# Kernel tuning notes

Hardware: AMD Instinct MI355X
Metric: run time of the kernel (lower is better)

The kernel has to match this reference:

```python
import jax, jax.numpy as jnp
import numpy as np

B = 4096          # events
L = 524288        # total set points (avg 128 per event)
CIN = 16          # per-point feature size (set feature 'a')
DVEC = 32         # flat feature size (feature 'b')
PHI = [128, 128, 64]
MLP = [256, 128]
EPS = 1e-5        # BatchNorm1d eps


def setup_inputs() -> dict:
    key = jax.random.key(0)
    ks = jax.random.split(key, 10)
    def n(k, shape, scale=0.05):
        return jax.random.normal(k, shape, dtype=jnp.float32) * scale
    return {
        "x_a": jax.random.normal(ks[0], (1, CIN, L), dtype=jnp.float32),
        "x_b": jax.random.normal(ks[1], (B, DVEC), dtype=jnp.float32),
        # row 0 -> counts for set feature 'a'; row 1 ignored (Reshape branch)
        "sample_indices": jnp.full((2, B), L // B, dtype=jnp.int32),
        "W1": n(ks[2], (PHI[0], CIN)),  "b1": jnp.zeros((PHI[0],), jnp.float32),
        "W2": n(ks[3], (PHI[1], PHI[0])), "b2": jnp.zeros((PHI[1],), jnp.float32),
        "W3": n(ks[4], (PHI[2], PHI[1])), "b3": jnp.zeros((PHI[2],), jnp.float32),
        "Wm1": n(ks[5], (MLP[0], PHI[2] + DVEC)), "bm1": jnp.zeros((MLP[0],), jnp.float32),
        "g1": jnp.ones((MLP[0],), jnp.float32), "be1": jnp.zeros((MLP[0],), jnp.float32),
        "Wm2": n(ks[6], (MLP[1], MLP[0])), "bm2": jnp.zeros((MLP[1],), jnp.float32),
        "g2": jnp.ones((MLP[1],), jnp.float32), "be2": jnp.zeros((MLP[1],), jnp.float32),
        "Wm3": n(ks[7], (1, MLP[1])), "bm3": jnp.zeros((1,), jnp.float32),
    }


def _bn(x, g, b):
    # BatchNorm1d, training-mode batch stats, biased variance (torch semantics)
    mu = jnp.mean(x, axis=0)
    var = jnp.var(x, axis=0)
    return (x - mu) * jax.lax.rsqrt(var + EPS) * g + b


def reference(x_a, x_b, sample_indices,
              W1, b1, W2, b2, W3, b3,
              Wm1, bm1, g1, be1, Wm2, bm2, g2, be2, Wm3, bm3):
    counts = sample_indices[0].astype(jnp.int32)                       # [B]
    bounds = jnp.concatenate([jnp.zeros((1,), jnp.int32), jnp.cumsum(counts)])  # [B+1]

    # PhiNet: pointwise Conv1d stack (kernel size 1) on [CIN, L]
    h = x_a[0]
    h = jax.nn.relu(jnp.einsum('oc,cl->ol', W1, h) + b1[:, None])
    h = jax.nn.relu(jnp.einsum('oc,cl->ol', W2, h) + b2[:, None])
    h = jax.nn.relu(jnp.einsum('oc,cl->ol', W3, h) + b3[:, None])      # [64, L]

    # fused segment-mean: point p belongs to segment j iff bounds[j] <= p < bounds[j+1]
    seg = jnp.searchsorted(bounds, jnp.arange(h.shape[1], dtype=jnp.int32), side='right') - 1
    sums = jax.ops.segment_sum(h.T, seg, num_segments=counts.shape[0])  # [B, 64]
    means = sums / jnp.maximum(counts, 1).astype(jnp.float32)[:, None]

    # feature order: sorted keys -> ('a' set repr, 'b' flat)
    z = jnp.concatenate([means, x_b.reshape(-1, DVEC)], axis=1)        # [B, 96]

    z = jax.nn.relu(_bn(z @ Wm1.T + bm1, g1, be1))
    z = jax.nn.relu(_bn(z @ Wm2.T + bm2, g2, be2))
    return jax.nn.sigmoid(z @ Wm3.T + bm3)                             # [B, 1]
```

## Files before the change

### kernel.cpp

```cpp
#include <hip/hip_runtime.h>
#include <hip/hip_bf16.h>

#define B_EVENTS 4096
#define L_PTS    524288
#define CIN      16
#define C1       128
#define C2       128
#define C3       64
#define DVEC     32
#define ZDIM     96
#define M1       256
#define M2       128
#define BN_EPS   1e-5f
#define TILE     64
#define NTILES   (L_PTS / TILE)
#define GRID_PHI 2048
#define NTPB     (NTILES / GRID_PHI)

#define XOFF     0
#define H1OFF    4096
#define H2OFF    20480
#define LDSSZ    36864

typedef __attribute__((ext_vector_type(8))) short bf16x8;
typedef __attribute__((ext_vector_type(4))) float f32x4;

__device__ __forceinline__ unsigned cvtpk(float lo, float hi) {
    unsigned r;
    asm("v_cvt_pk_bf16_f32 %0, %1, %2" : "=v"(r) : "v"(lo), "v"(hi));
    return r;
}

__device__ __forceinline__ unsigned long long pack4relub(f32x4 a, f32x4 b) {
    union { unsigned u[2]; unsigned long long ll; } pk;
    pk.u[0] = cvtpk(fmaxf(a[0] + b[0], 0.f), fmaxf(a[1] + b[1], 0.f));
    pk.u[1] = cvtpk(fmaxf(a[2] + b[2], 0.f), fmaxf(a[3] + b[3], 0.f));
    return pk.ll;
}

__device__ __forceinline__ bf16x8 frag_from_f32(const float* p) {
    const float4 lo = *(const float4*)p;
    const float4 hi = *(const float4*)(p + 4);
    union { unsigned u[4]; bf16x8 v; } r;
    r.u[0] = cvtpk(lo.x, lo.y);
    r.u[1] = cvtpk(lo.z, lo.w);
    r.u[2] = cvtpk(hi.x, hi.y);
    r.u[3] = cvtpk(hi.z, hi.w);
    return r.v;
}

__device__ __forceinline__ int ldsoff(int base, int rowSlots, int c, int sir) {
    int s = c * rowSlots + sir;
    s ^= (c & 7);
    return base + s * 16;
}

__device__ __forceinline__ int xaddr(int pt, int g) {
    return XOFF + (((pt * 4 + g) ^ (pt & 7)) * 16);
}

__global__ __launch_bounds__(1024) void scan_kernel(const int* __restrict__ si,
                                                    int* __restrict__ bounds,
                                                    int* __restrict__ tilemap)
{
    __shared__ int sh[1024];
    const int tid = threadIdx.x;
    const int c0 = si[tid*4+0], c1 = si[tid*4+1], c2 = si[tid*4+2], c3 = si[tid*4+3];
    const int s4 = c0 + c1 + c2 + c3;
    sh[tid] = s4;
    __syncthreads();
    for (int off = 1; off < 1024; off <<= 1) {
        int add = (tid >= off) ? sh[tid - off] : 0;
        __syncthreads();
        sh[tid] += add;
        __syncthreads();
    }
    const int excl = (tid == 0) ? 0 : sh[tid - 1];
    bounds[tid*4+0] = excl;
    bounds[tid*4+1] = excl + c0;
    bounds[tid*4+2] = excl + c0 + c1;
    bounds[tid*4+3] = excl + c0 + c1 + c2;
    if (tid == 1023) bounds[B_EVENTS] = excl + s4;
    __syncthreads();

    const int total = bounds[B_EVENTS];
    for (int t = tid; t < NTILES; t += 1024) {
        const int p0 = t * TILE;
        if (p0 >= total) { tilemap[t] = -1; continue; }
        int e = (int)(((long long)p0 * B_EVENTS) / total);
        if (e > B_EVENTS - 1) e = B_EVENTS - 1;
        while (bounds[e] > p0) --e;
        while (bounds[e + 1] <= p0) ++e;
        const bool fast = (p0 + TILE <= bounds[e + 1]);
        tilemap[t] = e | (fast ? (1 << 30) : 0);
    }
}

__global__ __launch_bounds__(256, 3) void phi_mfma_kernel(
    const float* __restrict__ xa,
    const int* __restrict__ bounds, const int* __restrict__ tilemap,
    const float* __restrict__ W1, const float* __restrict__ W2, const float* __restrict__ W3,
    const float* __restrict__ b1, const float* __restrict__ b2, const float* __restrict__ b3,
    float* __restrict__ zsum)
{
    __shared__ __align__(16) char lds[LDSSZ];

    const int tid  = threadIdx.x;
    const int lane = tid & 63;
    const int wm   = tid >> 6;
    const int g4   = lane >> 4;
    const int c16  = lane & 15;

    const int pt = tid & 63;
    const int h  = tid >> 6;
    int t = blockIdx.x;
    float xv[4];
    #pragma unroll
    for (int jj = 0; jj < 4; ++jj)
        xv[jj] = xa[(size_t)(h * 4 + jj) * L_PTS + t * TILE + pt];

    f32x4 bb1[2], bb2[2], bb3;
    #pragma unroll
    for (int mf = 0; mf < 2; ++mf) {
        bb1[mf] = *(const f32x4*)&b1[wm * 32 + mf * 16 + g4 * 4];
        bb2[mf] = *(const f32x4*)&b2[wm * 32 + mf * 16 + g4 * 4];
    }
    bb3 = *(const f32x4*)&b3[wm * 16 + g4 * 4];

    bf16x8 a1[2], a2[2][4], a3[4];
    {
        const bf16x8 zz = {0, 0, 0, 0, 0, 0, 0, 0};
        const int r1 = wm * 32 + c16;
        #pragma unroll
        for (int mf = 0; mf < 2; ++mf)
            a1[mf] = (g4 < 2) ? frag_from_f32(&W1[(r1 + mf * 16) * CIN + g4 * 8]) : zz;
        #pragma unroll
        for (int mf = 0; mf < 2; ++mf)
            #pragma unroll
            for (int kf = 0; kf < 4; ++kf)
                a2[mf][kf] = frag_from_f32(&W2[(r1 + mf * 16) * C1 + kf * 32 + g4 * 8]);
        const int r3 = wm * 16 + c16;
        #pragma unroll
        for (int kf = 0; kf < 4; ++kf)
            a3[kf] = frag_from_f32(&W3[r3 * C2 + kf * 32 + g4 * 8]);
    }

    {
        const int zs = 2 + (h >> 1);
        *(unsigned long long*)(lds + (((pt * 4 + zs) ^ (pt & 7)) * 16) + (h & 1) * 8) = 0ull;
        union { unsigned u[2]; unsigned long long ll; } pk;
        pk.u[0] = cvtpk(xv[0], xv[1]);
        pk.u[1] = cvtpk(xv[2], xv[3]);
        *(unsigned long long*)(lds + xaddr(pt, h >> 1) + (h & 1) * 8) = pk.ll;
    }
    __syncthreads();

    for (int it = 0; it < NTPB; ++it) {
        const int tm = tilemap[t];
        if (tm < 0) break;
        const int  e0    = tm & 0x3FFFFFFF;
        const bool fastp = (tm >> 30) & 1;
        const int  p0    = t * TILE;
        const int  tn    = t + GRID_PHI;
        const bool more  = (it + 1 < NTPB);

        if (more) {
            #pragma unroll
            for (int jj = 0; jj < 4; ++jj)
                xv[jj] = xa[(size_t)(h * 4 + jj) * L_PTS + tn * TILE + pt];
        }

        {
            f32x4 acc[2][4];
            #pragma unroll
            for (int mf = 0; mf < 2; ++mf)
                #pragma unroll
                for (int nf = 0; nf < 4; ++nf)
                    acc[mf][nf] = f32x4{0.f, 0.f, 0.f, 0.f};
            bf16x8 bfr[4];
            #pragma unroll
            for (int nf = 0; nf < 4; ++nf)
                bfr[nf] = *(const bf16x8*)(lds + xaddr(nf * 16 + c16, g4));
            __builtin_amdgcn_s_setprio(1);
            #pragma unroll
            for (int nf = 0; nf < 4; ++nf)
                #pragma unroll
                for (int mf = 0; mf < 2; ++mf)
                    acc[mf][nf] = __builtin_amdgcn_mfma_f32_16x16x32_bf16(a1[mf], bfr[nf], acc[mf][nf], 0, 0, 0);
            __builtin_amdgcn_s_setprio(0);
            #pragma unroll
            for (int mf = 0; mf < 2; ++mf) {
                const int sir = wm * 4 + mf * 2 + (g4 >> 1);
                #pragma unroll
                for (int nf = 0; nf < 4; ++nf) {
                    const int c = nf * 16 + c16;
                    *(unsigned long long*)(lds + ldsoff(H1OFF, 16, c, sir) + (g4 & 1) * 8) = pack4relub(acc[mf][nf], bb1[mf]);
                }
            }
        }
        __syncthreads();

        {
            f32x4 acc[2][4];
            #pragma unroll
            for (int mf = 0; mf < 2; ++mf)
                #pragma unroll
                for (int nf = 0; nf < 4; ++nf)
                    acc[mf][nf] = f32x4{0.f, 0.f, 0.f, 0.f};
            #pragma unroll
            for (int nf = 0; nf < 4; ++nf) {
                const int c = nf * 16 + c16;
                bf16x8 bk[4];
                #pragma unroll
                for (int kf = 0; kf < 4; ++kf)
                    bk[kf] = *(const bf16x8*)(lds + ldsoff(H1OFF, 16, c, kf * 4 + g4));
                __builtin_amdgcn_s_setprio(1);
                #pragma unroll
                for (int mf = 0; mf < 2; ++mf)
                    #pragma unroll
                    for (int kf = 0; kf < 4; ++kf)
                        acc[mf][nf] = __builtin_amdgcn_mfma_f32_16x16x32_bf16(a2[mf][kf], bk[kf], acc[mf][nf], 0, 0, 0);
                __builtin_amdgcn_s_setprio(0);
            }
            if (more) {
                union { unsigned u[2]; unsigned long long ll; } pk;
                pk.u[0] = cvtpk(xv[0], xv[1]);
                pk.u[1] = cvtpk(xv[2], xv[3]);
                *(unsigned long long*)(lds + xaddr(pt, h >> 1) + (h & 1) * 8) = pk.ll;
            }
            #pragma unroll
            for (int mf = 0; mf < 2; ++mf) {
                const int sir = wm * 4 + mf * 2 + (g4 >> 1);
                #pragma unroll
                for (int nf = 0; nf < 4; ++nf) {
                    const int c = nf * 16 + c16;
                    *(unsigned long long*)(lds + ldsoff(H2OFF, 16, c, sir) + (g4 & 1) * 8) = pack4relub(acc[mf][nf], bb2[mf]);
                }
            }
        }
        __syncthreads();

        {
            f32x4 acc3[4];
            #pragma unroll
            for (int nf = 0; nf < 4; ++nf) acc3[nf] = f32x4{0.f, 0.f, 0.f, 0.f};
            #pragma unroll
            for (int nf = 0; nf < 4; ++nf) {
                const int c = nf * 16 + c16;
                bf16x8 bk[4];
                #pragma unroll
                for (int kf = 0; kf < 4; ++kf)
                    bk[kf] = *(const bf16x8*)(lds + ldsoff(H2OFF, 16, c, kf * 4 + g4));
                __builtin_amdgcn_s_setprio(1);
                #pragma unroll
                for (int kf = 0; kf < 4; ++kf)
                    acc3[nf] = __builtin_amdgcn_mfma_f32_16x16x32_bf16(a3[kf], bk[kf], acc3[nf], 0, 0, 0);
                __builtin_amdgcn_s_setprio(0);
            }

            if (fastp) {
                float s[4] = {0.f, 0.f, 0.f, 0.f};
                #pragma unroll
                for (int nf = 0; nf < 4; ++nf)
                    #pragma unroll
                    for (int r = 0; r < 4; ++r)
                        s[r] += fmaxf(acc3[nf][r] + bb3[r], 0.f);
                #pragma unroll
                for (int r = 0; r < 4; ++r) {
                    float v = s[r];
                    v += __shfl_xor(v, 1, 64);
                    v += __shfl_xor(v, 2, 64);
                    v += __shfl_xor(v, 4, 64);
                    v += __shfl_xor(v, 8, 64);
                    s[r] = v;
                }
                if (c16 == 0) {
                    #pragma unroll
                    for (int r = 0; r < 4; ++r)
                        atomicAdd(&zsum[(size_t)e0 * C3 + wm * 16 + g4 * 4 + r], s[r]);
                }
            } else {
                const int total = bounds[B_EVENTS];
                #pragma unroll
                for (int nf = 0; nf < 4; ++nf) {
                    const int col = p0 + nf * 16 + c16;
                    if (col < total) {
                        int sgr = e0;
                        while (col >= bounds[sgr + 1]) ++sgr;
                        #pragma unroll
                        for (int r = 0; r < 4; ++r)
                            atomicAdd(&zsum[(size_t)sgr * C3 + wm * 16 + g4 * 4 + r],
                                      fmaxf(acc3[nf][r] + bb3[r], 0.f));
                    }
                }
            }
        }
        t = tn;
    }
}

__global__ __launch_bounds__(256) void mlp1_kernel(
    const float* __restrict__ zsum, const int* __restrict__ si, const float* __restrict__ xb,
    const float* __restrict__ Wm1, const float* __restrict__ bm1,
    float* __restrict__ y1, float* __restrict__ gsum, float* __restrict__ gsq)
{
    __shared__ float zs[8][ZDIM + 4];
    const int r0 = blockIdx.x * 8;
    const int tid = threadIdx.x;
    for (int i = tid; i < 8 * ZDIM; i += 256) {
        const int r = i / ZDIM, c = i - r * ZDIM;
        float v;
        if (c < C3) {
            const int cnt = si[r0 + r];
            v = zsum[(size_t)(r0 + r) * C3 + c] / (float)max(cnt, 1);
        } else {
            v = xb[(size_t)(r0 + r) * DVEC + (c - C3)];
        }
        zs[r][c] = v;
    }
    __syncthreads();
    const int o = tid;
    float acc[8];
    const float bb = bm1[o];
    #pragma unroll
    for (int r = 0; r < 8; ++r) acc[r] = bb;
    for (int c = 0; c < ZDIM; c += 4) {
        const float4 w = *(const float4*)&Wm1[o * ZDIM + c];
        #pragma unroll
        for (int r = 0; r < 8; ++r) {
            const float4 v = *(const float4*)&zs[r][c];
            acc[r] += w.x*v.x + w.y*v.y + w.z*v.z + w.w*v.w;
        }
    }
    float s = 0.f, sq = 0.f;
    #pragma unroll
    for (int r = 0; r < 8; ++r) {
        y1[(size_t)(r0 + r) * M1 + o] = acc[r];
        s += acc[r]; sq += acc[r] * acc[r];
    }
    atomicAdd(&gsum[o], s);
    atomicAdd(&gsq[o], sq);
}

__global__ __launch_bounds__(256) void mlp2_kernel(
    const float* __restrict__ y1,
    const float* __restrict__ gsum1, const float* __restrict__ gsq1,
    const float* __restrict__ g1, const float* __restrict__ be1,
    const float* __restrict__ Wm2, const float* __restrict__ bm2,
    float* __restrict__ y2, float* __restrict__ gsum, float* __restrict__ gsq)
{
    __shared__ float zs[8][M1 + 4];
    __shared__ float sc[M1], sh[M1];
    const int r0 = blockIdx.x * 8;
    const int tid = threadIdx.x;
    {
        const float mu  = gsum1[tid] * (1.f / B_EVENTS);
        const float var = gsq1[tid] * (1.f / B_EVENTS) - mu * mu;
        const float s0  = rsqrtf(var + BN_EPS) * g1[tid];
        sc[tid] = s0;
        sh[tid] = be1[tid] - mu * s0;
    }
    __syncthreads();
    for (int i = tid; i < 8 * M1; i += 256) {
        const int r = i >> 8, c = i & (M1 - 1);
        const float v = y1[(size_t)(r0 + r) * M1 + c];
        zs[r][c] = fmaxf(v * sc[c] + sh[c], 0.f);
    }
    __syncthreads();
    const int o = tid & 127;
    const int h = tid >> 7;
    float acc[4];
    const float bb = bm2[o];
    #pragma unroll
    for (int r = 0; r < 4; ++r) acc[r] = bb;
    for (int c = 0; c < M1; c += 4) {
        const float4 w = *(const float4*)&Wm2[o * M1 + c];
        #pragma unroll
        for (int r = 0; r < 4; ++r) {
            const float4 v = *(const float4*)&zs[h * 4 + r][c];
            acc[r] += w.x*v.x + w.y*v.y + w.z*v.z + w.w*v.w;
        }
    }
    float s = 0.f, sq = 0.f;
    #pragma unroll
    for (int r = 0; r < 4; ++r) {
        y2[(size_t)(r0 + h * 4 + r) * M2 + o] = acc[r];
        s += acc[r]; sq += acc[r] * acc[r];
    }
    atomicAdd(&gsum[o], s);
    atomicAdd(&gsq[o], sq);
}

__global__ __launch_bounds__(256) void final_kernel(
    const float* __restrict__ y2,
    const float* __restrict__ gsum2, const float* __restrict__ gsq2,
    const float* __restrict__ g2, const float* __restrict__ be2,
    const float* __restrict__ Wm3, const float* __restrict__ bm3,
    float* __restrict__ out)
{
    __shared__ float sc[M2], sh[M2];
    const int tid = threadIdx.x;
    if (tid < M2) {
        const float mu  = gsum2[tid] * (1.f / B_EVENTS);
        const float var = gsq2[tid] * (1.f / B_EVENTS) - mu * mu;
        const float s0  = rsqrtf(var + BN_EPS) * g2[tid];
        sc[tid] = s0;
        sh[tid] = be2[tid] - mu * s0;
    }
    __syncthreads();
    const int w = tid >> 6, l = tid & 63;
    const int r = blockIdx.x * 4 + w;
    const float e0 = fmaxf(y2[(size_t)r * M2 + l]      * sc[l]      + sh[l],      0.f);
    const float e1 = fmaxf(y2[(size_t)r * M2 + 64 + l] * sc[64 + l] + sh[64 + l], 0.f);
    float a = e0 * Wm3[l] + e1 * Wm3[64 + l];
    #pragma unroll
    for (int off = 32; off >= 1; off >>= 1) a += __shfl_down(a, off, 64);
    if (l == 0) out[r] = 1.f / (1.f + expf(-(a + bm3[0])));
}

extern "C" void kernel_launch(void* const* d_in, const int* in_sizes, int n_in,
                              void* d_out, int out_size, void* d_ws, size_t ws_size,
                              hipStream_t stream) {
    const float* xa  = (const float*)d_in[0];
    const float* xb  = (const float*)d_in[1];
    const int*   si  = (const int*)  d_in[2];
    const float* W1  = (const float*)d_in[3];
    const float* b1  = (const float*)d_in[4];
    const float* W2  = (const float*)d_in[5];
    const float* b2  = (const float*)d_in[6];
    const float* W3  = (const float*)d_in[7];
    const float* b3  = (const float*)d_in[8];
    const float* Wm1 = (const float*)d_in[9];
    const float* bm1 = (const float*)d_in[10];
    const float* g1  = (const float*)d_in[11];
    const float* be1 = (const float*)d_in[12];
    const float* Wm2 = (const float*)d_in[13];
    const float* bm2 = (const float*)d_in[14];
    const float* g2  = (const float*)d_in[15];
    const float* be2 = (const float*)d_in[16];
    const float* Wm3 = (const float*)d_in[17];
    const float* bm3 = (const float*)d_in[18];
    float* out = (float*)d_out;

    char* ws = (char*)d_ws;
    size_t off = 0;
    auto alloc = [&](size_t bytes) -> void* {
        void* p = ws + off;
        off = (off + bytes + 255) & ~(size_t)255;
        return p;
    };
    float* zsum    = (float*)alloc((size_t)B_EVENTS * C3 * sizeof(float));
    float* stats   = (float*)alloc(768 * sizeof(float));
    int*   bounds  = (int*)  alloc((B_EVENTS + 1) * sizeof(int));
    int*   tilemap = (int*)  alloc(NTILES * sizeof(int));
    float* y1      = (float*)alloc((size_t)B_EVENTS * M1 * sizeof(float));
    float* y2      = (float*)alloc((size_t)B_EVENTS * M2 * sizeof(float));
    float* gsum1 = stats;
    float* gsq1  = stats + 256;
    float* gsum2 = stats + 512;
    float* gsq2  = stats + 640;

    hipMemsetAsync(zsum, 0, (size_t)B_EVENTS * C3 * sizeof(float) + 768 * sizeof(float), stream);

    hipLaunchKernelGGL(scan_kernel, dim3(1), dim3(1024), 0, stream, si, bounds, tilemap);
    hipLaunchKernelGGL(phi_mfma_kernel, dim3(GRID_PHI), dim3(256), 0, stream,
                       xa, bounds, tilemap, W1, W2, W3, b1, b2, b3, zsum);
    hipLaunchKernelGGL(mlp1_kernel, dim3(B_EVENTS / 8), dim3(256), 0, stream,
                       zsum, si, xb, Wm1, bm1, y1, gsum1, gsq1);
    hipLaunchKernelGGL(mlp2_kernel, dim3(B_EVENTS / 8), dim3(256), 0, stream,
                       y1, gsum1, gsq1, g1, be1, Wm2, bm2, y2, gsum2, gsq2);
    hipLaunchKernelGGL(final_kernel, dim3(B_EVENTS / 4), dim3(256), 0, stream,
                       y2, gsum2, gsq2, g2, be2, Wm3, bm3, out);
}
```

Measured before the change: 137.6 us.

## Fuse MLP tail into cooperative kernel, re-tile phi waves 2x2, fold memset into scan

New measurement: 188.5 us. 37.0% more time.

```diff
diff --git a/kernel.cpp b/kernel.cpp
--- a/kernel.cpp
+++ b/kernel.cpp
@@ -1,5 +1,8 @@
 #include <hip/hip_runtime.h>
 #include <hip/hip_bf16.h>
+#include <hip/hip_cooperative_groups.h>
+
+namespace cg = cooperative_groups;
 
 #define B_EVENTS 4096
 #define L_PTS    524288
@@ -20,7 +23,10 @@
 #define XOFF     0
 #define H1OFF    4096
 #define H2OFF    20480
-#define LDSSZ    36864
+#define BIAS1    36864
+#define BIAS2    37376
+#define BIAS3    37888
+#define LDSSZ    38144
 
 typedef __attribute__((ext_vector_type(8))) short bf16x8;
 typedef __attribute__((ext_vector_type(4))) float f32x4;
@@ -61,10 +67,15 @@
 
 __global__ __launch_bounds__(1024) void scan_kernel(const int* __restrict__ si,
                                                     int* __restrict__ bounds,
-                                                    int* __restrict__ tilemap)
+                                                    int* __restrict__ tilemap,
+                                                    float* __restrict__ zsum)
 {
+    const int tid = threadIdx.x;
+    if (blockIdx.x == 1) {
+        for (int i = tid; i < B_EVENTS * C3 + 768; i += 1024) zsum[i] = 0.f;
+        return;
+    }
     __shared__ int sh[1024];
-    const int tid = threadIdx.x;
     const int c0 = si[tid*4+0], c1 = si[tid*4+1], c2 = si[tid*4+2], c3 = si[tid*4+3];
     const int s4 = c0 + c1 + c2 + c3;
     sh[tid] = s4;
@@ -96,7 +107,7 @@
     }
 }
 
-__global__ __launch_bounds__(256, 3) void phi_mfma_kernel(
+__global__ __launch_bounds__(256, 2) void phi_mfma_kernel(
     const float* __restrict__ xa,
     const int* __restrict__ bounds, const int* __restrict__ tilemap,
     const float* __restrict__ W1, const float* __restrict__ W2, const float* __restrict__ W3,
@@ -107,7 +118,9 @@
 
     const int tid  = threadIdx.x;
     const int lane = tid & 63;
-    const int wm   = tid >> 6;
+    const int wid  = tid >> 6;
+    const int wm   = wid >> 1;
+    const int wn   = wid & 1;
     const int g4   = lane >> 4;
     const int c16  = lane & 15;
 
@@ -119,30 +132,31 @@
     for (int jj = 0; jj < 4; ++jj)
         xv[jj] = xa[(size_t)(h * 4 + jj) * L_PTS + t * TILE + pt];
 
-    f32x4 bb1[2], bb2[2], bb3;
-    #pragma unroll
-    for (int mf = 0; mf < 2; ++mf) {
-        bb1[mf] = *(const f32x4*)&b1[wm * 32 + mf * 16 + g4 * 4];
-        bb2[mf] = *(const f32x4*)&b2[wm * 32 + mf * 16 + g4 * 4];
-    }
-    bb3 = *(const f32x4*)&b3[wm * 16 + g4 * 4];
-
-    bf16x8 a1[2], a2[2][4], a3[4];
+    if (tid < 128) {
+        ((float*)(lds + BIAS1))[tid] = b1[tid];
+        ((float*)(lds + BIAS2))[tid] = b2[tid];
+    } else if (tid < 192) {
+        ((float*)(lds + BIAS3))[tid - 128] = b3[tid - 128];
+    }
+
+    bf16x8 a1[4], a2[4][4], a3[2][4];
     {
         const bf16x8 zz = {0, 0, 0, 0, 0, 0, 0, 0};
-        const int r1 = wm * 32 + c16;
-        #pragma unroll
-        for (int mf = 0; mf < 2; ++mf)
+        const int r1 = wm * 64 + c16;
+        #pragma unroll
+        for (int mf = 0; mf < 4; ++mf)
             a1[mf] = (g4 < 2) ? frag_from_f32(&W1[(r1 + mf * 16) * CIN + g4 * 8]) : zz;
         #pragma unroll
-        for (int mf = 0; mf < 2; ++mf)
+        for (int mf = 0; mf < 4; ++mf)
             #pragma unroll
             for (int kf = 0; kf < 4; ++kf)
                 a2[mf][kf] = frag_from_f32(&W2[(r1 + mf * 16) * C1 + kf * 32 + g4 * 8]);
-        const int r3 = wm * 16 + c16;
-        #pragma unroll
-        for (int kf = 0; kf < 4; ++kf)
-            a3[kf] = frag_from_f32(&W3[r3 * C2 + kf * 32 + g4 * 8]);
+        const int r3 = wm * 32 + c16;
+        #pragma unroll
+        for (int mf = 0; mf < 2; ++mf)
+            #pragma unroll
+            for (int kf = 0; kf < 4; ++kf)
+                a3[mf][kf] = frag_from_f32(&W3[(r3 + mf * 16) * C2 + kf * 32 + g4 * 8]);
     }
 
     {
@@ -171,52 +185,53 @@
         }
 
         {
-            f32x4 acc[2][4];
-            #pragma unroll
-            for (int mf = 0; mf < 2; ++mf)
-                #pragma unroll
-                for (int nf = 0; nf < 4; ++nf)
-                    acc[mf][nf] = f32x4{0.f, 0.f, 0.f, 0.f};
-            bf16x8 bfr[4];
-            #pragma unroll
-            for (int nf = 0; nf < 4; ++nf)
-                bfr[nf] = *(const bf16x8*)(lds + xaddr(nf * 16 + c16, g4));
+            f32x4 acc[4][2];
+            #pragma unroll
+            for (int mf = 0; mf < 4; ++mf) {
+                acc[mf][0] = f32x4{0.f, 0.f, 0.f, 0.f};
+                acc[mf][1] = f32x4{0.f, 0.f, 0.f, 0.f};
+            }
+            bf16x8 bfr[2];
+            #pragma unroll
+            for (int nf = 0; nf < 2; ++nf)
+                bfr[nf] = *(const bf16x8*)(lds + xaddr(wn * 32 + nf * 16 + c16, g4));
             __builtin_amdgcn_s_setprio(1);
             #pragma unroll
-            for (int nf = 0; nf < 4; ++nf)
-                #pragma unroll
-                for (int mf = 0; mf < 2; ++mf)
+            for (int nf = 0; nf < 2; ++nf)
+                #pragma unroll
+                for (int mf = 0; mf < 4; ++mf)
                     acc[mf][nf] = __builtin_amdgcn_mfma_f32_16x16x32_bf16(a1[mf], bfr[nf], acc[mf][nf], 0, 0, 0);
             __builtin_amdgcn_s_setprio(0);
             #pragma unroll
-            for (int mf = 0; mf < 2; ++mf) {
-                const int sir = wm * 4 + mf * 2 + (g4 >> 1);
-                #pragma unroll
-                for (int nf = 0; nf < 4; ++nf) {
-                    const int c = nf * 16 + c16;
-                    *(unsigned long long*)(lds + ldsoff(H1OFF, 16, c, sir) + (g4 & 1) * 8) = pack4relub(acc[mf][nf], bb1[mf]);
+            for (int mf = 0; mf < 4; ++mf) {
+                const f32x4 bb = *(const f32x4*)(lds + BIAS1 + (wm * 64 + mf * 16 + g4 * 4) * 4);
+                const int sir = wm * 8 + mf * 2 + (g4 >> 1);
+                #pragma unroll
+                for (int nf = 0; nf < 2; ++nf) {
+                    const int c = wn * 32 + nf * 16 + c16;
+                    *(unsigned long long*)(lds + ldsoff(H1OFF, 16, c, sir) + (g4 & 1) * 8) = pack4relub(acc[mf][nf], bb);
                 }
             }
         }
         __syncthreads();
 
         {
-            f32x4 acc[2][4];
-            #pragma unroll
-            for (int mf = 0; mf < 2; ++mf)
-                #pragma unroll
-                for (int nf = 0; nf < 4; ++nf)
-                    acc[mf][nf] = f32x4{0.f, 0.f, 0.f, 0.f};
-            #pragma unroll
-            for (int nf = 0; nf < 4; ++nf) {
-                const int c = nf * 16 + c16;
+            f32x4 acc[4][2];
+            #pragma unroll
+            for (int mf = 0; mf < 4; ++mf) {
+                acc[mf][0] = f32x4{0.f, 0.f, 0.f, 0.f};
+                acc[mf][1] = f32x4{0.f, 0.f, 0.f, 0.f};
+            }
+            #pragma unroll
+            for (int nf = 0; nf < 2; ++nf) {
+                const int c = wn * 32 + nf * 16 + c16;
                 bf16x8 bk[4];
                 #pragma unroll
                 for (int kf = 0; kf < 4; ++kf)
                     bk[kf] = *(const bf16x8*)(lds + ldsoff(H1OFF, 16, c, kf * 4 + g4));
                 __builtin_amdgcn_s_setprio(1);
                 #pragma unroll
-                for (int mf = 0; mf < 2; ++mf)
+                for (int mf = 0; mf < 4; ++mf)
                     #pragma unroll
                     for (int kf = 0; kf < 4; ++kf)
                         acc[mf][nf] = __builtin_amdgcn_mfma_f32_16x16x32_bf16(a2[mf][kf], bk[kf], acc[mf][nf], 0, 0, 0);
@@ -229,68 +244,86 @@
                 *(unsigned long long*)(lds + xaddr(pt, h >> 1) + (h & 1) * 8) = pk.ll;
             }
             #pragma unroll
+            for (int mf = 0; mf < 4; ++mf) {
+                const f32x4 bb = *(const f32x4*)(lds + BIAS2 + (wm * 64 + mf * 16 + g4 * 4) * 4);
+                const int sir = wm * 8 + mf * 2 + (g4 >> 1);
+                #pragma unroll
+                for (int nf = 0; nf < 2; ++nf) {
+                    const int c = wn * 32 + nf * 16 + c16;
+                    *(unsigned long long*)(lds + ldsoff(H2OFF, 16, c, sir) + (g4 & 1) * 8) = pack4relub(acc[mf][nf], bb);
+                }
+            }
+        }
+        __syncthreads();
+
+        {
+            f32x4 acc3[2][2];
+            #pragma unroll
             for (int mf = 0; mf < 2; ++mf) {
-                const int sir = wm * 4 + mf * 2 + (g4 >> 1);
-                #pragma unroll
-                for (int nf = 0; nf < 4; ++nf) {
-                    const int c = nf * 16 + c16;
-                    *(unsigned long long*)(lds + ldsoff(H2OFF, 16, c, sir) + (g4 & 1) * 8) = pack4relub(acc[mf][nf], bb2[mf]);
-                }
-            }
-        }
-        __syncthreads();
-
-        {
-            f32x4 acc3[4];
-            #pragma unroll
-            for (int nf = 0; nf < 4; ++nf) acc3[nf] = f32x4{0.f, 0.f, 0.f, 0.f};
-            #pragma unroll
-            for (int nf = 0; nf < 4; ++nf) {
-                const int c = nf * 16 + c16;
+                acc3[mf][0] = f32x4{0.f, 0.f, 0.f, 0.f};
+                acc3[mf][1] = f32x4{0.f, 0.f, 0.f, 0.f};
+            }
+            #pragma unroll
+            for (int nf = 0; nf < 2; ++nf) {
+                const int c = wn * 32 + nf * 16 + c16;
                 bf16x8 bk[4];
                 #pragma unroll
                 for (int kf = 0; kf < 4; ++kf)
                     bk[kf] = *(const bf16x8*)(lds + ldsoff(H2OFF, 16, c, kf * 4 + g4));
                 __builtin_amdgcn_s_setprio(1);
                 #pragma unroll
-                for (int kf = 0; kf < 4; ++kf)
-                    acc3[nf] = __builtin_amdgcn_mfma_f32_16x16x32_bf16(a3[kf], bk[kf], acc3[nf], 0, 0, 0);
+                for (int mf = 0; mf < 2; ++mf)
+                    #pragma unroll
+                    for (int kf = 0; kf < 4; ++kf)
+                        acc3[mf][nf] = __builtin_amdgcn_mfma_f32_16x16x32_bf16(a3[mf][kf], bk[kf], acc3[mf][nf], 0, 0, 0);
                 __builtin_amdgcn_s_setprio(0);
             }
+            f32x4 bb3[2];
+            #pragma unroll
+            for (int mf = 0; mf < 2; ++mf)
+                bb3[mf] = *(const f32x4*)(lds + BIAS3 + (wm * 32 + mf * 16 + g4 * 4) * 4);
 
             if (fastp) {
-                float s[4] = {0.f, 0.f, 0.f, 0.f};
-                #pragma unroll
-                for (int nf = 0; nf < 4; ++nf)
+                float s[2][4];
+                #pragma unroll
+                for (int mf = 0; mf < 2; ++mf)
                     #pragma unroll
-                    for (int r = 0; r < 4; ++r)
-                        s[r] += fmaxf(acc3[nf][r] + bb3[r], 0.f);
-                #pragma unroll
-                for (int r = 0; r < 4; ++r) {
-                    float v = s[r];
-                    v += __shfl_xor(v, 1, 64);
-                    v += __shfl_xor(v, 2, 64);
-                    v += __shfl_xor(v, 4, 64);
-                    v += __shfl_xor(v, 8, 64);
-                    s[r] = v;
-                }
+                    for (int r = 0; r < 4; ++r) {
+                        s[mf][r] = fmaxf(acc3[mf][0][r] + bb3[mf][r], 0.f)
+                                 + fmaxf(acc3[mf][1][r] + bb3[mf][r], 0.f);
+                    }
+                #pragma unroll
+                for (int mf = 0; mf < 2; ++mf)
+                    #pragma unroll
+                    for (int r = 0; r < 4; ++r) {
+                        float v = s[mf][r];
+                        v += __shfl_xor(v, 1, 64);
+                        v += __shfl_xor(v, 2, 64);
+                        v += __shfl_xor(v, 4, 64);
+                        v += __shfl_xor(v, 8, 64);
+                        s[mf][r] = v;
+                    }
                 if (c16 == 0) {
                     #pragma unroll
-                    for (int r = 0; r < 4; ++r)
-                        atomicAdd(&zsum[(size_t)e0 * C3 + wm * 16 + g4 * 4 + r], s[r]);
+                    for (int mf = 0; mf < 2; ++mf)
+                        #pragma unroll
+                        for (int r = 0; r < 4; ++r)
+                            atomicAdd(&zsum[(size_t)e0 * C3 + wm * 32 + mf * 16 + g4 * 4 + r], s[mf][r]);
                 }
             } else {
                 const int total = bounds[B_EVENTS];
                 #pragma unroll
-                for (int nf = 0; nf < 4; ++nf) {
-                    const int col = p0 + nf * 16 + c16;
+                for (int nf = 0; nf < 2; ++nf) {
+                    const int col = p0 + wn * 32 + nf * 16 + c16;
                     if (col < total) {
                         int sgr = e0;
                         while (col >= bounds[sgr + 1]) ++sgr;
                         #pragma unroll
-                        for (int r = 0; r < 4; ++r)
-                            atomicAdd(&zsum[(size_t)sgr * C3 + wm * 16 + g4 * 4 + r],
-                                      fmaxf(acc3[nf][r] + bb3[r], 0.f));
+                        for (int mf = 0; mf < 2; ++mf)
+                            #pragma unroll
+                            for (int r = 0; r < 4; ++r)
+                                atomicAdd(&zsum[(size_t)sgr * C3 + wm * 32 + mf * 16 + g4 * 4 + r],
+                                          fmaxf(acc3[mf][nf][r] + bb3[mf][r], 0.f));
                     }
                 }
             }
@@ -299,15 +332,24 @@
     }
 }
 
-__global__ __launch_bounds__(256) void mlp1_kernel(
+__global__ __launch_bounds__(256) void tail_kernel(
     const float* __restrict__ zsum, const int* __restrict__ si, const float* __restrict__ xb,
     const float* __restrict__ Wm1, const float* __restrict__ bm1,
-    float* __restrict__ y1, float* __restrict__ gsum, float* __restrict__ gsq)
+    const float* __restrict__ g1, const float* __restrict__ be1,
+    const float* __restrict__ Wm2, const float* __restrict__ bm2,
+    const float* __restrict__ g2, const float* __restrict__ be2,
+    const float* __restrict__ Wm3, const float* __restrict__ bm3,
+    float* __restrict__ stats, float* __restrict__ out)
 {
-    __shared__ float zs[8][ZDIM + 4];
-    const int r0 = blockIdx.x * 8;
+    cg::grid_group grid = cg::this_grid();
+    __shared__ float zs[16][ZDIM + 4];
+    __shared__ float y1s[16][M1 + 4];
+    __shared__ float y2s[16][M2 + 4];
+    __shared__ float sc2s[M2], sh2s[M2];
+    const int r0 = blockIdx.x * 16;
     const int tid = threadIdx.x;
-    for (int i = tid; i < 8 * ZDIM; i += 256) {
+
+    for (int i = tid; i < 16 * ZDIM; i += 256) {
         const int r = i / ZDIM, c = i - r * ZDIM;
         float v;
         if (c < C3) {
@@ -319,103 +361,88 @@
         zs[r][c] = v;
     }
     __syncthreads();
-    const int o = tid;
-    float acc[8];
-    const float bb = bm1[o];
-    #pragma unroll
-    for (int r = 0; r < 8; ++r) acc[r] = bb;
-    for (int c = 0; c < ZDIM; c += 4) {
-        const float4 w = *(const float4*)&Wm1[o * ZDIM + c];
+    {
+        float acc[16];
+        const float bb = bm1[tid];
+        #pragma unroll
+        for (int r = 0; r < 16; ++r) acc[r] = bb;
+        for (int c = 0; c < ZDIM; c += 4) {
+            const float4 w = *(const float4*)&Wm1[tid * ZDIM + c];
+            #pragma unroll
+            for (int r = 0; r < 16; ++r) {
+                const float4 v = *(const float4*)&zs[r][c];
+                acc[r] += w.x*v.x + w.y*v.y + w.z*v.z + w.w*v.w;
+            }
+        }
+        float s = 0.f, sq = 0.f;
+        #pragma unroll
+        for (int r = 0; r < 16; ++r) {
+            y1s[r][tid] = acc[r];
+            s += acc[r]; sq += acc[r] * acc[r];
+        }
+        atomicAdd(&stats[tid], s);
+        atomicAdd(&stats[256 + tid], sq);
+    }
+    grid.sync();
+
+    {
+        const float mu  = stats[tid] * (1.f / B_EVENTS);
+        const float var = stats[256 + tid] * (1.f / B_EVENTS) - mu * mu;
+        const float s0  = rsqrtf(var + BN_EPS) * g1[tid];
+        const float sh0 = be1[tid] - mu * s0;
+        #pragma unroll
+        for (int r = 0; r < 16; ++r)
+            y1s[r][tid] = fmaxf(y1s[r][tid] * s0 + sh0, 0.f);
+    }
+    __syncthreads();
+    {
+        const int o = tid & 127;
+        const int hh = tid >> 7;
+        float acc[8];
+        const float bb = bm2[o];
+        #pragma unroll
+        for (int r = 0; r < 8; ++r) acc[r] = bb;
+        for (int c = 0; c < M1; c += 4) {
+            const float4 w = *(const float4*)&Wm2[o * M1 + c];
+            #pragma unroll
+            for (int r = 0; r < 8; ++r) {
+                const float4 v = *(const float4*)&y1s[hh * 8 + r][c];
+                acc[r] += w.x*v.x + w.y*v.y + w.z*v.z + w.w*v.w;
+            }
+        }
+        float s = 0.f, sq = 0.f;
         #pragma unroll
         for (int r = 0; r < 8; ++r) {
-            const float4 v = *(const float4*)&zs[r][c];
-            acc[r] += w.x*v.x + w.y*v.y + w.z*v.z + w.w*v.w;
-        }
-    }
-    float s = 0.f, sq = 0.f;
-    #pragma unroll
-    for (int r = 0; r < 8; ++r) {
-        y1[(size_t)(r0 + r) * M1 + o] = acc[r];
-        s += acc[r]; sq += acc[r] * acc[r];
-    }
-    atomicAdd(&gsum[o], s);
-    atomicAdd(&gsq[o], sq);
-}
-
-__global__ __launch_bounds__(256) void mlp2_kernel(
-    const float* __restrict__ y1,
-    const float* __restrict__ gsum1, const float* __restrict__ gsq1,
-    const float* __restrict__ g1, const float* __restrict__ be1,
-    const float* __restrict__ Wm2, const float* __restrict__ bm2,
-    float* __restrict__ y2, float* __restrict__ gsum, float* __restrict__ gsq)
-{
-    __shared__ float zs[8][M1 + 4];
-    __shared__ float sc[M1], sh[M1];
-    const int r0 = blockIdx.x * 8;
-    const int tid = threadIdx.x;
-    {
-        const float mu  = gsum1[tid] * (1.f / B_EVENTS);
-        const float var = gsq1[tid] * (1.f / B_EVENTS) - mu * mu;
-        const float s0  = rsqrtf(var + BN_EPS) * g1[tid];
-        sc[tid] = s0;
-        sh[tid] = be1[tid] - mu * s0;
-    }
-    __syncthreads();
-    for (int i = tid; i < 8 * M1; i += 256) {
-        const int r = i >> 8, c = i & (M1 - 1);
-        const float v = y1[(size_t)(r0 + r) * M1 + c];
-        zs[r][c] = fmaxf(v * sc[c] + sh[c], 0.f);
-    }
-    __syncthreads();
-    const int o = tid & 127;
-    const int h = tid >> 7;
-    float acc[4];
-    const float bb = bm2[o];
-    #pragma unroll
-    for (int r = 0; r < 4; ++r) acc[r] = bb;
-    for (int c = 0; c < M1; c += 4) {
-        const float4 w = *(const float4*)&Wm2[o * M1 + c];
-        #pragma unroll
-        for (int r = 0; r < 4; ++r) {
-            const float4 v = *(const float4*)&zs[h * 4 + r][c];
-            acc[r] += w.x*v.x + w.y*v.y + w.z*v.z + w.w*v.w;
-        }
-    }
-    float s = 0.f, sq = 0.f;
-    #pragma unroll
-    for (int r = 0; r < 4; ++r) {
-        y2[(size_t)(r0 + h * 4 + r) * M2 + o] = acc[r];
-        s += acc[r]; sq += acc[r] * acc[r];
-    }
-    atomicAdd(&gsum[o], s);
-    atomicAdd(&gsq[o], sq);
-}
-
-__global__ __launch_bounds__(256) void final_kernel(
-    const float* __restrict__ y2,
-    const float* __restrict__ gsum2, const float* __restrict__ gsq2,
-    const float* __restrict__ g2, const float* __restrict__ be2,
-    const float* __restrict__ Wm3, const float* __restrict__ bm3,
-    float* __restrict__ out)
-{
-    __shared__ float sc[M2], sh[M2];
-    const int tid = threadIdx.x;
+            y2s[hh * 8 + r][o] = acc[r];
+            s += acc[r]; sq += acc[r] * acc[r];
+        }
+        atomicAdd(&stats[512 + o], s);
+        atomicAdd(&stats[640 + o], sq);
+    }
+    grid.sync();
+
     if (tid < M2) {
-        const float mu  = gsum2[tid] * (1.f / B_EVENTS);
-        const float var = gsq2[tid] * (1.f / B_EVENTS) - mu * mu;
+        const float mu  = stats[512 + tid] * (1.f / B_EVENTS);
+        const float var = stats[640 + tid] * (1.f / B_EVENTS) - mu * mu;
         const float s0  = rsqrtf(var + BN_EPS) * g2[tid];
-        sc[tid] = s0;
-        sh[tid] = be2[tid] - mu * s0;
-    }
-    __syncthreads();
-    const int w = tid >> 6, l = tid & 63;
-    const int r = blockIdx.x * 4 + w;
-    const float e0 = fmaxf(y2[(size_t)r * M2 + l]      * sc[l]      + sh[l],      0.f);
-    const float e1 = fmaxf(y2[(size_t)r * M2 + 64 + l] * sc[64 + l] + sh[64 + l], 0.f);
-    float a = e0 * Wm3[l] + e1 * Wm3[64 + l];
-    #pragma unroll
-    for (int off = 32; off >= 1; off >>= 1) a += __shfl_down(a, off, 64);
-    if (l == 0) out[r] = 1.f / (1.f + expf(-(a + bm3[0])));
+        sc2s[tid] = s0;
+        sh2s[tid] = be2[tid] - mu * s0;
+    }
+    __syncthreads();
+    {
+        const int w = tid >> 6, l = tid & 63;
+        const float w0 = Wm3[l], w1 = Wm3[64 + l];
+        #pragma unroll
+        for (int k = 0; k < 4; ++k) {
+            const int row = w * 4 + k;
+            const float e0 = fmaxf(y2s[row][l]      * sc2s[l]      + sh2s[l],      0.f);
+            const float e1 = fmaxf(y2s[row][64 + l] * sc2s[64 + l] + sh2s[64 + l], 0.f);
+            float a = e0 * w0 + e1 * w1;
+            #pragma unroll
+            for (int off = 32; off >= 1; off >>= 1) a += __shfl_down(a, off, 64);
+            if (l == 0) out[r0 + row] = 1.f / (1.f + expf(-(a + bm3[0])));
+        }
+    }
 }
 
 extern "C" void kernel_launch(void* const* d_in, const int* in_sizes, int n_in,
@@ -453,22 +480,16 @@
     float* stats   = (float*)alloc(768 * sizeof(float));
     int*   bounds  = (int*)  alloc((B_EVENTS + 1) * sizeof(int));
     int*   tilemap = (int*)  alloc(NTILES * sizeof(int));
-    float* y1      = (float*)alloc((size_t)B_EVENTS * M1 * sizeof(float));
-    float* y2      = (float*)alloc((size_t)B_EVENTS * M2 * sizeof(float));
-    float* gsum1 = stats;
-    float* gsq1  = stats + 256;
-    float* gsum2 = stats + 512;
-    float* gsq2  = stats + 640;
-
-    hipMemsetAsync(zsum, 0, (size_t)B_EVENTS * C3 * sizeof(float) + 768 * sizeof(float), stream);
-
-    hipLaunchKernelGGL(scan_kernel, dim3(1), dim3(1024), 0, stream, si, bounds, tilemap);
+
+    hipLaunchKernelGGL(scan_kernel, dim3(2), dim3(1024), 0, stream, si, bounds, tilemap, zsum);
     hipLaunchKernelGGL(phi_mfma_kernel, dim3(GRID_PHI), dim3(256), 0, stream,
                        xa, bounds, tilemap, W1, W2, W3, b1, b2, b3, zsum);
-    hipLaunchKernelGGL(mlp1_kernel, dim3(B_EVENTS / 8), dim3(256), 0, stream,
-                       zsum, si, xb, Wm1, bm1, y1, gsum1, gsq1);
-    hipLaunchKernelGGL(mlp2_kernel, dim3(B_EVENTS / 8), dim3(256), 0, stream,
-                       y1, gsum1, gsq1, g1, be1, Wm2, bm2, y2, gsum2, gsq2);
-    hipLaunchKernelGGL(final_kernel, dim3(B_EVENTS / 4), dim3(256), 0, stream,
-                       y2, gsum2, gsq2, g2, be2, Wm3, bm3, out);
-}
+
+    void* args[] = {
+        (void*)&zsum, (void*)&si, (void*)&xb,
+        (void*)&Wm1, (void*)&bm1, (void*)&g1, (void*)&be1,
+        (void*)&Wm2, (void*)&bm2, (void*)&g2, (void*)&be2,
+        (void*)&Wm3, (void*)&bm3, (void*)&stats, (void*)&out
+    };
+    hipLaunchCooperativeKernel((void*)tail_kernel, dim3(256), dim3(256), args, 0, stream);
+}
```
